# Kernel tuning notes

Measured on AMD Instinct MI355X. Metric: run time of the kernel, lower is better.

## Reference

```python
import jax, jax.numpy as jnp
import numpy as np

B, M, C, D, H, W = 2, 4, 32, 32, 32, 32
E, O = 4, 128
MC = M * C
BN_EPS = 1e-5


def setup_inputs() -> dict:
    key = jax.random.key(0)
    ks = jax.random.split(key, 8)
    inp = {
        "f0": jax.random.normal(ks[0], (B, C, D, H, W), jnp.float32),
        "f1": jax.random.normal(ks[1], (B, C, D, H, W), jnp.float32),
        "f2": jax.random.normal(ks[2], (B, C, D, H, W), jnp.float32),
        "f3": jax.random.normal(ks[3], (B, C, D, H, W), jnp.float32),
        # per-expert 1x1x1 conv weights [E, O, MC] (bias=False)
        "Wc": jax.random.normal(ks[4], (E, O, MC), jnp.float32) * 0.05,
        # BatchNorm3d params (eval mode), per expert per out-channel
        "gamma": jnp.ones((E, O), jnp.float32),
        "beta": jnp.zeros((E, O), jnp.float32),
        "rmean": jnp.zeros((E, O), jnp.float32),
        "rvar": jnp.ones((E, O), jnp.float32),
        # router Linear(MC -> E)
        "Wr": jax.random.normal(ks[5], (E, MC), jnp.float32) * 0.02,
        "br": jnp.zeros((E,), jnp.float32),
        "top_k": 2,
    }
    return inp


def reference(f0, f1, f2, f3, Wc, gamma, beta, rmean, rvar, Wr, br, top_k):
    x = jnp.concatenate([f0, f1, f2, f3], axis=1)          # [B, MC, D, H, W]
    Bn, MCn, Dn, Hn, Wn = x.shape
    En = Wr.shape[0]

    # router: global average pool -> linear -> softmax -> top-k
    pooled = x.mean(axis=(2, 3, 4))                        # [B, MC]
    logits = pooled @ Wr.T + br                            # [B, E]
    probs = jax.nn.softmax(logits, axis=-1)
    topk_vals, topk_idx = jax.lax.top_k(probs, top_k)      # [B, k]
    topk_w = topk_vals / topk_vals.sum(axis=-1, keepdims=True)

    # auxiliary load-balancing loss (top-1 one-hot)
    one_hot = jax.nn.one_hot(topk_idx[:, 0], En, dtype=probs.dtype)
    f_e = one_hot.mean(axis=0)
    p_e = probs.mean(axis=0)
    aux_loss = En * (f_e * p_e).sum()

    # all experts: 1x1x1 conv == channel GEMM, then eval-mode BN + ReLU
    xs = x.reshape(Bn, MCn, -1)                            # [B, MC, S]
    y = jnp.einsum('eoc,bcs->ebos', Wc, xs)                # [E, B, O, S]
    inv = gamma * jax.lax.rsqrt(rvar + BN_EPS)             # [E, O]
    y = y * inv[:, None, :, None] + (beta - rmean * inv)[:, None, :, None]
    y = jax.nn.relu(y)

    # dispatch/combine: per-sample expert weights scattered to [B, E]
    cw = jnp.zeros((Bn, En), x.dtype).at[
        jnp.arange(Bn)[:, None], topk_idx
    ].add(topk_w)
    out = jnp.einsum('be,ebos->bos', cw, y).reshape(Bn, -1, Dn, Hn, Wn)
    return out, aux_loss
```

## Files before the change

kernel.cpp:

```cpp
#include <hip/hip_runtime.h>
#include <stdint.h>

#define S_TOT 32768
#define MC_DIM 128
#define O_DIM 128
#define BN_EPS 1e-5f
#define S_TILE 128

#define WS_PART  0
#define WS_BIAS  512
#define WS_W2    1024

typedef __attribute__((ext_vector_type(8))) short short8;
typedef __attribute__((ext_vector_type(4))) float f32x4;

static __device__ __forceinline__ unsigned short f2bf(float f) {
    union { float f; unsigned int u; } v; v.f = f;
    unsigned int r = v.u + 0x7FFFu + ((v.u >> 16) & 1u);
    return (unsigned short)(r >> 16);
}

__global__ __launch_bounds__(256) void k_pool(
    const float* __restrict__ f0, const float* __restrict__ f1,
    const float* __restrict__ f2, const float* __restrict__ f3,
    const float* __restrict__ Wc, const float* __restrict__ gamma,
    const float* __restrict__ beta, const float* __restrict__ rmean,
    const float* __restrict__ rvar, float* __restrict__ ws) {

    __shared__ float red[256];
    int bid = blockIdx.x;
    int half = bid >> 8, ch = bid & 255;
    int b = ch >> 7, c = ch & 127;
    int t = threadIdx.x;

    if (t < 32) {
        int i = bid * 32 + t;
        int eo = i >> 5;
        float inv = gamma[eo] * rsqrtf(rvar[eo] + BN_EPS);
        float4 w = ((const float4*)Wc)[i];
        uint2 pk;
        pk.x = (unsigned int)f2bf(w.x * inv) | ((unsigned int)f2bf(w.y * inv) << 16);
        pk.y = (unsigned int)f2bf(w.z * inv) | ((unsigned int)f2bf(w.w * inv) << 16);
        ((uint2*)(ws + WS_W2))[i] = pk;
    } else if (t == 32) {
        float inv = gamma[bid] * rsqrtf(rvar[bid] + BN_EPS);
        ws[WS_BIAS + bid] = beta[bid] - rmean[bid] * inv;
    }

    const float* fp = (c < 32) ? f0 : (c < 64) ? f1 : (c < 96) ? f2 : f3;
    const float4* base = (const float4*)(fp + ((size_t)b * 32 + (c & 31)) * S_TOT + half * 16384);
    float s = 0.f;
    #pragma unroll
    for (int j = 0; j < 16; ++j) {
        float4 v = base[j * 256 + t];
        s += (v.x + v.y) + (v.z + v.w);
    }
    red[t] = s;
    __syncthreads();
    #pragma unroll
    for (int off = 128; off > 0; off >>= 1) {
        if (t < off) red[t] += red[t + off];
        __syncthreads();
    }
    if (t == 0) ws[WS_PART + half * 256 + ch] = red[0];
}

__global__ __launch_bounds__(256, 2) void k_moe(
    const float* __restrict__ f0, const float* __restrict__ f1,
    const float* __restrict__ f2, const float* __restrict__ f3,
    const float* __restrict__ Wr, const float* __restrict__ br,
    const float* __restrict__ ws, float* __restrict__ out) {

    __shared__ uint4 tile4[2048];
    __shared__ float pooled[256];
    __shared__ int   route_e[2];
    __shared__ float route_w[2];
    char* lds = (char*)tile4;

    int bid = blockIdx.x;
    int b = bid >> 8;
    int st = bid & 255;
    int s0 = st * S_TILE;
    int t = threadIdx.x;

    #pragma unroll
    for (int i = 0; i < 16; ++i) {
        int lin = i * 256 + t;
        int c = lin >> 5;
        int sq = lin & 31;
        const float* fp = (c < 32) ? f0 : (c < 64) ? f1 : (c < 96) ? f2 : f3;
        float4 v = *(const float4*)(fp + ((size_t)b * 32 + (c & 31)) * S_TOT + s0 + sq * 4);
        int cpart = ((c >> 3) << 4) ^ 0;
        int clow = (c & 7) * 2;
        int s = sq * 4;
        *(unsigned short*)(lds + (s + 0) * 256 + (cpart ^ (((s + 0) & 15) << 4)) + clow) = f2bf(v.x);
        *(unsigned short*)(lds + (s + 1) * 256 + (cpart ^ (((s + 1) & 15) << 4)) + clow) = f2bf(v.y);
        *(unsigned short*)(lds + (s + 2) * 256 + (cpart ^ (((s + 2) & 15) << 4)) + clow) = f2bf(v.z);
        *(unsigned short*)(lds + (s + 3) * 256 + (cpart ^ (((s + 3) & 15) << 4)) + clow) = f2bf(v.w);
    }

    pooled[t] = ws[WS_PART + t] + ws[WS_PART + 256 + t];
    __syncthreads();
    if (t < 64) {
        int l = t;
        const float s_inv = 1.0f / (float)S_TOT;
        float x0 = pooled[l] * s_inv;
        float x1 = pooled[64 + l] * s_inv;
        float y0 = pooled[128 + l] * s_inv;
        float y1 = pooled[192 + l] * s_inv;
        float lg[8];
        #pragma unroll
        for (int e = 0; e < 4; ++e) {
            float wc0 = Wr[e * MC_DIM + l];
            float wc1 = Wr[e * MC_DIM + 64 + l];
            lg[e] = x0 * wc0 + x1 * wc1;
            lg[4 + e] = y0 * wc0 + y1 * wc1;
        }
        #pragma unroll
        for (int msk = 32; msk >= 1; msk >>= 1) {
            #pragma unroll
            for (int e = 0; e < 8; ++e) lg[e] += __shfl_xor(lg[e], msk);
        }
        if (l == 0) {
            float probs[2][4];
            int top1[2];
            #pragma unroll
            for (int bb = 0; bb < 2; ++bb) {
                float lo[4];
                for (int e = 0; e < 4; ++e) lo[e] = lg[bb * 4 + e] + br[e];
                float mx = fmaxf(fmaxf(lo[0], lo[1]), fmaxf(lo[2], lo[3]));
                float sum = 0.f;
                for (int e = 0; e < 4; ++e) { probs[bb][e] = expf(lo[e] - mx); sum += probs[bb][e]; }
                for (int e = 0; e < 4; ++e) probs[bb][e] /= sum;
                int e0 = 0; float v0 = probs[bb][0];
                for (int e = 1; e < 4; ++e) if (probs[bb][e] > v0) { v0 = probs[bb][e]; e0 = e; }
                int e1 = -1; float v1 = -1.f;
                for (int e = 0; e < 4; ++e) if (e != e0 && probs[bb][e] > v1) { v1 = probs[bb][e]; e1 = e; }
                top1[bb] = e0;
                if (bb == b) {
                    float inv = 1.f / (v0 + v1);
                    route_e[0] = e0; route_e[1] = e1;
                    route_w[0] = v0 * inv; route_w[1] = v1 * inv;
                }
            }
            if (bid == 0) {
                float aux = 0.f;
                for (int e = 0; e < 4; ++e) {
                    float fe = 0.5f * ((top1[0] == e) + (top1[1] == e));
                    float pe = 0.5f * (probs[0][e] + probs[1][e]);
                    aux += fe * pe;
                }
                out[(size_t)8388608] = 4.f * aux;
            }
        }
    }
    __syncthreads();

    int e0 = route_e[0], e1 = route_e[1];
    float w0 = route_w[0], w1 = route_w[1];
    const unsigned short* W2 = (const unsigned short*)(ws + WS_W2);
    const float* bias2 = ws + WS_BIAS;

    int wv = t >> 6, l = t & 63;
    int o0 = wv * 32;
    int lr = l & 15, lg2 = l >> 4;

    f32x4 acc[2][2][8];
    #pragma unroll
    for (int ee = 0; ee < 2; ++ee)
        #pragma unroll
        for (int of = 0; of < 2; ++of)
            #pragma unroll
            for (int sf = 0; sf < 8; ++sf)
                acc[ee][of][sf] = (f32x4){0.f, 0.f, 0.f, 0.f};

    #pragma unroll
    for (int kk = 0; kk < 4; ++kk) {
        short8 a[2][2];
        #pragma unroll
        for (int ee = 0; ee < 2; ++ee) {
            int e = ee ? e1 : e0;
            #pragma unroll
            for (int of = 0; of < 2; ++of) {
                int o = o0 + of * 16 + lr;
                a[ee][of] = *(const short8*)(W2 + ((size_t)(e * O_DIM + o) * MC_DIM + kk * 32 + lg2 * 8));
            }
        }
        #pragma unroll
        for (int sf = 0; sf < 8; ++sf) {
            int sl = sf * 16 + lr;
            int gr = kk * 4 + lg2;
            int byte = sl * 256 + ((gr ^ lr) << 4);
            short8 bb = *(const short8*)(lds + byte);
            #pragma unroll
            for (int ee = 0; ee < 2; ++ee)
                #pragma unroll
                for (int of = 0; of < 2; ++of)
                    acc[ee][of][sf] = __builtin_amdgcn_mfma_f32_16x16x32_bf16(
                        a[ee][of], bb, acc[ee][of][sf], 0, 0, 0);
        }
    }

    #pragma unroll
    for (int of = 0; of < 2; ++of) {
        #pragma unroll
        for (int r = 0; r < 4; ++r) {
            int o = o0 + of * 16 + lg2 * 4 + r;
            float bA = bias2[e0 * O_DIM + o];
            float bB = bias2[e1 * O_DIM + o];
            float* orow = out + ((size_t)(b * O_DIM + o)) * S_TOT + s0;
            #pragma unroll
            for (int sf = 0; sf < 8; ++sf) {
                float y0 = fmaxf(acc[0][of][sf][r] + bA, 0.f);
                float y1 = fmaxf(acc[1][of][sf][r] + bB, 0.f);
                orow[sf * 16 + lr] = w0 * y0 + w1 * y1;
            }
        }
    }
}

extern "C" void kernel_launch(void* const* d_in, const int* in_sizes, int n_in,
                              void* d_out, int out_size, void* d_ws, size_t ws_size,
                              hipStream_t stream) {
    const float* f0    = (const float*)d_in[0];
    const float* f1    = (const float*)d_in[1];
    const float* f2    = (const float*)d_in[2];
    const float* f3    = (const float*)d_in[3];
    const float* Wc    = (const float*)d_in[4];
    const float* gamma = (const float*)d_in[5];
    const float* beta  = (const float*)d_in[6];
    const float* rmean = (const float*)d_in[7];
    const float* rvar  = (const float*)d_in[8];
    const float* Wr    = (const float*)d_in[9];
    const float* br    = (const float*)d_in[10];
    float* ws  = (float*)d_ws;
    float* out = (float*)d_out;

    hipLaunchKernelGGL(k_pool, dim3(512), dim3(256), 0, stream,
                       f0, f1, f2, f3, Wc, gamma, beta, rmean, rvar, ws);
    hipLaunchKernelGGL(k_moe, dim3(512), dim3(256), 0, stream,
                       f0, f1, f2, f3, Wr, br, ws, out);
}
```

Baseline: 32.32 us.

## Fuse pooling into MoE kernel with grid-wide atomic barrier

Merges the separate pooling kernel into the main MoE kernel. Each block computes per-channel partial sums from the tile it already loads, adds them atomically into workspace, then spins on a global counter until all 512 blocks arrive before computing routing. This removes the second full read of the input and one kernel launch, but adds a memset launch and a software grid barrier. The barrier relies on all 512 blocks being co-resident, and the atomic float adds make the pooled sums order-dependent.

```diff
diff --git a/kernel.cpp b/kernel.cpp
--- a/kernel.cpp
+++ b/kernel.cpp
@@ -7,9 +7,10 @@
 #define BN_EPS 1e-5f
 #define S_TILE 128
 
-#define WS_PART  0
-#define WS_BIAS  512
-#define WS_W2    1024
+#define WS_CNT   0
+#define WS_PART2 16
+#define WS_BIAS  4608
+#define WS_W2    5120
 
 typedef __attribute__((ext_vector_type(8))) short short8;
 typedef __attribute__((ext_vector_type(4))) float f32x4;
@@ -20,17 +21,26 @@
     return (unsigned short)(r >> 16);
 }
 
-__global__ __launch_bounds__(256) void k_pool(
+__global__ __launch_bounds__(256, 2) void k_all(
     const float* __restrict__ f0, const float* __restrict__ f1,
     const float* __restrict__ f2, const float* __restrict__ f3,
     const float* __restrict__ Wc, const float* __restrict__ gamma,
     const float* __restrict__ beta, const float* __restrict__ rmean,
-    const float* __restrict__ rvar, float* __restrict__ ws) {
-
-    __shared__ float red[256];
+    const float* __restrict__ rvar, const float* __restrict__ Wr,
+    const float* __restrict__ br, float* __restrict__ ws,
+    float* __restrict__ out) {
+
+    __shared__ uint4 tile4[2048];
+    __shared__ float lds_pool[128];
+    __shared__ float pooled[256];
+    __shared__ int   route_e[2];
+    __shared__ float route_w[2];
+    char* lds = (char*)tile4;
+
     int bid = blockIdx.x;
-    int half = bid >> 8, ch = bid & 255;
-    int b = ch >> 7, c = ch & 127;
+    int b = bid >> 8;
+    int st = bid & 255;
+    int s0 = st * S_TILE;
     int t = threadIdx.x;
 
     if (t < 32) {
@@ -47,42 +57,6 @@
         ws[WS_BIAS + bid] = beta[bid] - rmean[bid] * inv;
     }
 
-    const float* fp = (c < 32) ? f0 : (c < 64) ? f1 : (c < 96) ? f2 : f3;
-    const float4* base = (const float4*)(fp + ((size_t)b * 32 + (c & 31)) * S_TOT + half * 16384);
-    float s = 0.f;
-    #pragma unroll
-    for (int j = 0; j < 16; ++j) {
-        float4 v = base[j * 256 + t];
-        s += (v.x + v.y) + (v.z + v.w);
-    }
-    red[t] = s;
-    __syncthreads();
-    #pragma unroll
-    for (int off = 128; off > 0; off >>= 1) {
-        if (t < off) red[t] += red[t + off];
-        __syncthreads();
-    }
-    if (t == 0) ws[WS_PART + half * 256 + ch] = red[0];
-}
-
-__global__ __launch_bounds__(256, 2) void k_moe(
-    const float* __restrict__ f0, const float* __restrict__ f1,
-    const float* __restrict__ f2, const float* __restrict__ f3,
-    const float* __restrict__ Wr, const float* __restrict__ br,
-    const float* __restrict__ ws, float* __restrict__ out) {
-
-    __shared__ uint4 tile4[2048];
-    __shared__ float pooled[256];
-    __shared__ int   route_e[2];
-    __shared__ float route_w[2];
-    char* lds = (char*)tile4;
-
-    int bid = blockIdx.x;
-    int b = bid >> 8;
-    int st = bid & 255;
-    int s0 = st * S_TILE;
-    int t = threadIdx.x;
-
     #pragma unroll
     for (int i = 0; i < 16; ++i) {
         int lin = i * 256 + t;
@@ -90,17 +64,44 @@
         int sq = lin & 31;
         const float* fp = (c < 32) ? f0 : (c < 64) ? f1 : (c < 96) ? f2 : f3;
         float4 v = *(const float4*)(fp + ((size_t)b * 32 + (c & 31)) * S_TOT + s0 + sq * 4);
-        int cpart = ((c >> 3) << 4) ^ 0;
+        int cpart = (c >> 3) << 4;
         int clow = (c & 7) * 2;
         int s = sq * 4;
         *(unsigned short*)(lds + (s + 0) * 256 + (cpart ^ (((s + 0) & 15) << 4)) + clow) = f2bf(v.x);
         *(unsigned short*)(lds + (s + 1) * 256 + (cpart ^ (((s + 1) & 15) << 4)) + clow) = f2bf(v.y);
         *(unsigned short*)(lds + (s + 2) * 256 + (cpart ^ (((s + 2) & 15) << 4)) + clow) = f2bf(v.z);
         *(unsigned short*)(lds + (s + 3) * 256 + (cpart ^ (((s + 3) & 15) << 4)) + clow) = f2bf(v.w);
-    }
-
-    pooled[t] = ws[WS_PART + t] + ws[WS_PART + 256 + t];
-    __syncthreads();
+        float p = (v.x + v.y) + (v.z + v.w);
+        #pragma unroll
+        for (int msk = 16; msk >= 1; msk >>= 1) p += __shfl_xor(p, msk, 32);
+        if ((t & 31) == 0) lds_pool[c] = p;
+    }
+    __syncthreads();
+
+    if (t < 128)
+        atomicAdd(&ws[WS_PART2 + ((b * 16 + (st >> 4)) * 128) + t], lds_pool[t]);
+    __syncthreads();
+
+    int* cnt = (int*)ws + WS_CNT;
+    if (t == 0) {
+        __threadfence();
+        atomicAdd(cnt, 1);
+        while (__hip_atomic_load(cnt, __ATOMIC_ACQUIRE, __HIP_MEMORY_SCOPE_AGENT) < 512)
+            __builtin_amdgcn_s_sleep(2);
+    }
+    __syncthreads();
+    __threadfence();
+
+    {
+        int bb = t >> 7, c = t & 127;
+        float s = 0.f;
+        #pragma unroll
+        for (int r = 0; r < 16; ++r)
+            s += ws[WS_PART2 + ((bb * 16 + r) * 128) + c];
+        pooled[t] = s;
+    }
+    __syncthreads();
+
     if (t < 64) {
         int l = t;
         const float s_inv = 1.0f / (float)S_TOT;
@@ -236,8 +237,7 @@
     float* ws  = (float*)d_ws;
     float* out = (float*)d_out;
 
-    hipLaunchKernelGGL(k_pool, dim3(512), dim3(256), 0, stream,
-                       f0, f1, f2, f3, Wc, gamma, beta, rmean, rvar, ws);
-    hipLaunchKernelGGL(k_moe, dim3(512), dim3(256), 0, stream,
-                       f0, f1, f2, f3, Wr, br, ws, out);
+    hipMemsetAsync(d_ws, 0, (16 + 2 * 16 * 128) * sizeof(float), stream);
+    hipLaunchKernelGGL(k_all, dim3(512), dim3(256), 0, stream,
+                       f0, f1, f2, f3, Wc, gamma, beta, rmean, rvar, Wr, br, ws, out);
 }
```

Result: slower. 100.7 us (+211.7%).
